# Optimization experiments

Measured on AMD Instinct MI355X. Metric: run time of the kernel, lower is better.

The kernel has to match this reference:

```python
import jax, jax.numpy as jnp
import numpy as np

NEG_INF = -1e30


def setup_inputs() -> dict:
    key = jax.random.key(0)
    kx, km, kq, kk, kv, ko = jax.random.split(key, 6)
    B, D, L = 2, 1024, 2048
    H, DK = 16, 64
    x = jax.random.normal(kx, (B, D, L), dtype=jnp.float32)
    mask = (jax.random.uniform(km, (B, L)) < 0.9).astype(jnp.float32)
    # per-head projection weights, stacked: (H, D, DK); output proj (D, H*DK)==(D, D)
    sq = 1.0 / np.sqrt(D)
    Wq = jax.random.normal(kq, (H, D, DK), dtype=jnp.float32) * sq
    Wk = jax.random.normal(kk, (H, D, DK), dtype=jnp.float32) * sq
    Wv = jax.random.normal(kv, (H, D, DK), dtype=jnp.float32) * sq
    Wo = jax.random.normal(ko, (D, H * DK), dtype=jnp.float32) * sq
    return {"x": x, "mask": mask, "Wq": Wq, "Wk": Wk, "Wv": Wv, "Wo": Wo}


def reference(x, mask, Wq, Wk, Wv, Wo):
    # x: (B, D, L); original transposes to (B, L, D)
    B, D, L = x.shape
    H, _, DK = Wq.shape
    xt = jnp.transpose(x, (0, 2, 1))  # (B, L, D)
    q = jnp.einsum('bld,hdk->bhlk', xt, Wq)
    k = jnp.einsum('bld,hdk->bhlk', xt, Wk)
    v = jnp.einsum('bld,hdk->bhlk', xt, Wv)
    scores = jnp.einsum('bhlk,bhmk->bhlm', q, k) * (1.0 / np.sqrt(DK))
    # masked log-softmax over keys (hmask), squad-style: mask*logit + (1-mask)*-1e30
    hmask = mask[:, None, None, :]  # (B,1,1,Lk)
    masked = hmask * scores + (1.0 - hmask) * NEG_INF
    logp = jax.nn.log_softmax(masked, axis=-1)
    # second softmax over the log-probs, then multiplicative vmask on query dim
    p = jax.nn.softmax(logp, axis=-1) * mask[:, None, :, None]
    heads = jnp.einsum('bhlm,bhmk->bhlk', p, v)  # (B,H,L,DK)
    head = jnp.transpose(heads, (0, 2, 1, 3)).reshape(B, L, H * DK)
    out = jnp.einsum('ble,de->bld', head, Wo)  # matmul(head, Wo) with Wo (D, H*DK)... 
    # NOTE: torch.matmul(head, Wo) treats Wo as (H*DK_in, D_out) only if square; here
    # Wo is (D, H*DK) with D == H*DK, and torch contracts head's last dim with Wo's FIRST dim:
    out = head @ Wo  # (B, L, H*DK) @ (D, H*DK) requires D==H*DK; contracts dim 0 of Wo
    return jnp.transpose(out, (0, 2, 1))  # (B, D, L)


if __name__ == "__main__":
    print(reference(**setup_inputs()).shape)
```

## Files before the change

kernel.cpp:

```cpp
#include <hip/hip_runtime.h>
#include <hip/hip_bf16.h>

typedef unsigned short u16;
typedef unsigned int u32;
typedef unsigned long long u64;
typedef short s8v __attribute__((ext_vector_type(8)));
typedef __bf16 bfv8 __attribute__((ext_vector_type(8)));
typedef float f4 __attribute__((ext_vector_type(4)));
typedef u64 u64v2 __attribute__((ext_vector_type(2)));

static constexpr int B = 2, D = 1024, L = 2048, H = 16, DK = 64, E = 1024;
static constexpr float QSCALE = 0.125f * 1.44269504088896340736f;
static constexpr float SMB = -16.0f;

#define DEV __device__ __forceinline__

DEV u16 f2bf(float f) {
  unsigned int u = __float_as_uint(f);
  u += 0x7FFFu + ((u >> 16) & 1u);
  return (u16)(u >> 16);
}
DEV float fexp2(float x) { return __builtin_amdgcn_exp2f(x); }
DEV u32 pkbf(float a, float b) {
  __hip_bfloat162 h = __float22bfloat162_rn(float2{a, b});
  u32 r;
  __builtin_memcpy(&r, &h, 4);
  return r;
}

#define GLD_LDS16(gp, lp)                                                     \
  __builtin_amdgcn_global_load_lds(                                           \
      (const __attribute__((address_space(1))) void*)(gp),                    \
      (__attribute__((address_space(3))) void*)(lp), 16, 0, 0)

__global__ __launch_bounds__(256) void k_prep(
    const float* __restrict__ x, const float* __restrict__ Wq,
    const float* __restrict__ Wk, const float* __restrict__ Wv,
    const float* __restrict__ Wo, u16* __restrict__ xt, u16* __restrict__ Wt,
    u16* __restrict__ WoT) {
  __shared__ u16 t[64][67];
  const int tid = threadIdx.x;
  const int g = blockIdx.x;
  const float* src;
  u16* dst;
  int sld, dld;
  if (g < 1024) {
    const int b = g >> 9, dt = (g >> 5) & 15, lt = g & 31;
    src = x + ((size_t)b * D + dt * 64) * L + lt * 64;
    sld = L;
    dst = xt + ((size_t)b * L + lt * 64) * D + dt * 64;
    dld = D;
  } else if (g < 1792) {
    const int u = g - 1024;
    const int w = u >> 8, h = (u >> 4) & 15, dt = u & 15;
    const float* Ws = (w == 0) ? Wq : ((w == 1) ? Wk : Wv);
    src = Ws + ((size_t)h * D + dt * 64) * DK;
    sld = DK;
    dst = Wt + ((size_t)(w * H + h) * DK) * D + dt * 64;
    dld = D;
  } else {
    const int v = g - 1792;
    const int et = v >> 4, dt = v & 15;
    src = Wo + ((size_t)et * 64) * D + dt * 64;
    sld = D;
    dst = WoT + ((size_t)dt * 64) * E + et * 64;
    dld = E;
  }
  const int r = tid >> 2, c16 = (tid & 3) * 16;
#pragma unroll
  for (int j = 0; j < 16; j += 4) {
    const f4 v4 = *(const f4*)(src + (size_t)r * sld + c16 + j);
    t[r][c16 + j]     = f2bf(v4[0]);
    t[r][c16 + j + 1] = f2bf(v4[1]);
    t[r][c16 + j + 2] = f2bf(v4[2]);
    t[r][c16 + j + 3] = f2bf(v4[3]);
  }
  __syncthreads();
  s8v o0, o1;
#pragma unroll
  for (int i = 0; i < 8; ++i) {
    o0[i] = (short)t[c16 + i][r];
    o1[i] = (short)t[c16 + 8 + i][r];
  }
  *(s8v*)(dst + (size_t)r * dld + c16)     = o0;
  *(s8v*)(dst + (size_t)r * dld + c16 + 8) = o1;
}

template <int AR>
DEV void gemm_tile(const u16* __restrict__ A, const u16* __restrict__ Bt,
                   int arow0, int brow0, u16* As, u16* Bs,
                   f4 (&acc)[AR / 32][4]) {
  const int tid = threadIdx.x;
  const int wid = tid >> 6, lane = tid & 63;
  const int q = lane >> 4, ln = lane & 15;
  const int wr = wid >> 1, wc = wid & 1;
  const int lrow = lane >> 2;
  const int lcg = (lane & 3) ^ ((lane >> 3) & 3);
  const int scA = (q ^ ((ln >> 1) & 3)) * 8;
  constexpr int MT = AR / 32;

  for (int k0 = 0; k0 < 1024; k0 += 32) {
    __syncthreads();
#pragma unroll
    for (int j = 0; j < AR / 64; ++j) {
      const int rb = wid * (AR / 4) + j * 16;
      const u16* gp = A + (size_t)(arow0 + rb + lrow) * 1024 + k0 + lcg * 8;
      GLD_LDS16(gp, As + rb * 32);
    }
#pragma unroll
    for (int j = 0; j < 2; ++j) {
      const int rb = wid * 32 + j * 16;
      const u16* gp = Bt + (size_t)(brow0 + rb + lrow) * 1024 + k0 + lcg * 8;
      GLD_LDS16(gp, Bs + rb * 32);
    }
    __syncthreads();
    bfv8 af[MT], bf[4];
#pragma unroll
    for (int mt = 0; mt < MT; ++mt)
      af[mt] = *(const bfv8*)(As + (wr * (AR / 2) + mt * 16 + ln) * 32 + scA);
#pragma unroll
    for (int nt = 0; nt < 4; ++nt)
      bf[nt] = *(const bfv8*)(Bs + (wc * 64 + nt * 16 + ln) * 32 + scA);
#pragma unroll
    for (int mt = 0; mt < MT; ++mt)
#pragma unroll
      for (int nt = 0; nt < 4; ++nt)
        acc[mt][nt] = __builtin_amdgcn_mfma_f32_16x16x32_bf16(
            af[mt], bf[nt], acc[mt][nt], 0, 0, 0);
  }
}

__global__ __launch_bounds__(256, 3) void k_qkvg(
    const u16* __restrict__ xt, const u16* __restrict__ Wt,
    u16* __restrict__ Q, u16* __restrict__ K, u16* __restrict__ Vt) {
  __shared__ u16 As[128 * 32];
  __shared__ u16 Bs[128 * 32];
  const int bm = blockIdx.x, bn = blockIdx.y;
  f4 acc[4][4];
#pragma unroll
  for (int mt = 0; mt < 4; ++mt)
#pragma unroll
    for (int nt = 0; nt < 4; ++nt) acc[mt][nt] = (f4){0.f, 0.f, 0.f, 0.f};
  gemm_tile<128>(xt, Wt, bm * 128, bn * 128, As, Bs, acc);

  const int tid = threadIdx.x, wid = tid >> 6, lane = tid & 63;
  const int q = lane >> 4, ln = lane & 15;
  const int wr = wid >> 1, wc = wid & 1;
  const int h2 = bn * 2 + wc;
  const int wsel = h2 >> 4, h = h2 & 15;
  const int b = bm >> 4;
  const int lbase = (bm & 15) * 128 + wr * 64;
  if (wsel == 0) {
    u16* dst = Q + (size_t)(b * H + h) * L * DK;
#pragma unroll
    for (int mt = 0; mt < 4; ++mt)
#pragma unroll
      for (int nt = 0; nt < 4; ++nt)
#pragma unroll
        for (int r = 0; r < 4; ++r)
          dst[(size_t)(lbase + mt * 16 + q * 4 + r) * DK + nt * 16 + ln] =
              f2bf(acc[mt][nt][r] * QSCALE);
  } else if (wsel == 1) {
    u16* dst = K + (size_t)(b * H + h) * L * DK;
#pragma unroll
    for (int mt = 0; mt < 4; ++mt)
#pragma unroll
      for (int nt = 0; nt < 4; ++nt)
#pragma unroll
        for (int r = 0; r < 4; ++r)
          dst[(size_t)(lbase + mt * 16 + q * 4 + r) * DK + nt * 16 + ln] =
              f2bf(acc[mt][nt][r]);
  } else {
    u16* dst = Vt + (size_t)(b * H + h) * DK * L;
#pragma unroll
    for (int mt = 0; mt < 4; ++mt)
#pragma unroll
      for (int nt = 0; nt < 4; ++nt)
#pragma unroll
        for (int r = 0; r < 4; ++r) {
          const int l = lbase + mt * 16 + q * 4 + r;
          dst[(size_t)(nt * 16 + ln) * L + (l & ~63) + ((l & 15) << 2) +
              ((l >> 4) & 3)] = f2bf(acc[mt][nt][r]);
        }
  }
}

__global__ __launch_bounds__(256, 2) void k_attn(
    const u16* __restrict__ Q, const u16* __restrict__ K,
    const u16* __restrict__ Vt, const float* __restrict__ mask,
    u16* __restrict__ Hd) {
  __shared__ u16 kt[64 * 64];
  __shared__ u16 vt[64 * 64];
  __shared__ float mf[L];
  __shared__ u16 p_lds[4][32 * 72];
  const int lt = blockIdx.x, h = blockIdx.y, b = blockIdx.z;
  const int tid = threadIdx.x;
  const int w = tid >> 6, lane = tid & 63, q = lane >> 4, ln = lane & 15;
  for (int i = tid; i < L; i += 256) mf[i] = mask[(size_t)b * L + i];

  const int bh = b * H + h;
  const u16* Qp = Q + (size_t)bh * L * DK;
  const u16* Kp = K + (size_t)bh * L * DK;
  const u16* Vp = Vt + (size_t)bh * DK * L;
  const int lq = lt * 128 + w * 32;

  bfv8 qf[2][2];
#pragma unroll
  for (int mt = 0; mt < 2; ++mt) {
    qf[mt][0] = *(const bfv8*)(Qp + (size_t)(lq + mt * 16 + ln) * DK + q * 8);
    qf[mt][1] =
        *(const bfv8*)(Qp + (size_t)(lq + mt * 16 + ln) * DK + 32 + q * 8);
  }

  f4 o[2][4];
  float l_r[2][4];
#pragma unroll
  for (int mt = 0; mt < 2; ++mt)
#pragma unroll
    for (int i = 0; i < 4; ++i) {
      o[mt][i] = (f4){0.f, 0.f, 0.f, 0.f};
      l_r[mt][i] = 0.f;
    }
  u16* pw = &p_lds[w][0];

  const int lrow = lane >> 3;
  const int lc = (lane & 7) ^ lrow;
  const int fr0 = w * 16 + lrow, fr1 = w * 16 + 8 + lrow;
  const int c0 = (q ^ (ln & 7)) * 8;
  const int c1 = ((q + 4) ^ (ln & 7)) * 8;

  for (int m0 = 0; m0 < L; m0 += 64) {
    __syncthreads();
    GLD_LDS16(Kp + (size_t)(m0 + fr0) * DK + lc * 8, kt + (w * 16) * 64);
    GLD_LDS16(Kp + (size_t)(m0 + fr1) * DK + lc * 8, kt + (w * 16 + 8) * 64);
    GLD_LDS16(Vp + (size_t)fr0 * L + m0 + lc * 8, vt + (w * 16) * 64);
    GLD_LDS16(Vp + (size_t)fr1 * L + m0 + lc * 8, vt + (w * 16 + 8) * 64);
    __syncthreads();

    float km[4];
    f4 s[2][4];
#pragma unroll
    for (int nt = 0; nt < 4; ++nt) {
      const int row = nt * 16 + ln;
      const bfv8 kf0 = *(const bfv8*)(kt + row * 64 + c0);
      const bfv8 kf1 = *(const bfv8*)(kt + row * 64 + c1);
      km[nt] = mf[m0 + row];
#pragma unroll
      for (int mt = 0; mt < 2; ++mt) {
        f4 a = (f4){SMB, SMB, SMB, SMB};
        a = __builtin_amdgcn_mfma_f32_16x16x32_bf16(qf[mt][0], kf0, a, 0, 0, 0);
        a = __builtin_amdgcn_mfma_f32_16x16x32_bf16(qf[mt][1], kf1, a, 0, 0, 0);
        s[mt][nt] = a;
      }
    }
#pragma unroll
    for (int mt = 0; mt < 2; ++mt)
#pragma unroll
      for (int r = 0; r < 4; ++r) {
        const float p0 = fexp2(s[mt][0][r]) * km[0];
        const float p1 = fexp2(s[mt][1][r]) * km[1];
        const float p2 = fexp2(s[mt][2][r]) * km[2];
        const float p3 = fexp2(s[mt][3][r]) * km[3];
        l_r[mt][r] += (p0 + p1) + (p2 + p3);
        const u64 pk = (u64)pkbf(p0, p1) | ((u64)pkbf(p2, p3) << 32);
        *(u64*)(pw + (mt * 16 + q * 4 + r) * 72 + ln * 4) = pk;
      }
    bfv8 pa[2][2];
#pragma unroll
    for (int mt = 0; mt < 2; ++mt) {
      u64v2 r0, r1;
      r0[0] = *(const u64*)(pw + (mt * 16 + ln) * 72 + q * 8);
      r0[1] = *(const u64*)(pw + (mt * 16 + ln) * 72 + q * 8 + 4);
      r1[0] = *(const u64*)(pw + (mt * 16 + ln) * 72 + 32 + q * 8);
      r1[1] = *(const u64*)(pw + (mt * 16 + ln) * 72 + 32 + q * 8 + 4);
      pa[mt][0] = __builtin_bit_cast(bfv8, r0);
      pa[mt][1] = __builtin_bit_cast(bfv8, r1);
    }
#pragma unroll
    for (int nt = 0; nt < 4; ++nt) {
      const int row = nt * 16 + ln;
      const bfv8 vf0 = *(const bfv8*)(vt + row * 64 + c0);
      const bfv8 vf1 = *(const bfv8*)(vt + row * 64 + c1);
#pragma unroll
      for (int mt = 0; mt < 2; ++mt) {
        o[mt][nt] = __builtin_amdgcn_mfma_f32_16x16x32_bf16(pa[mt][0], vf0,
                                                            o[mt][nt], 0, 0, 0);
        o[mt][nt] = __builtin_amdgcn_mfma_f32_16x16x32_bf16(pa[mt][1], vf1,
                                                            o[mt][nt], 0, 0, 0);
      }
    }
  }
#pragma unroll
  for (int mt = 0; mt < 2; ++mt)
#pragma unroll
    for (int r = 0; r < 4; ++r) {
#pragma unroll
      for (int off = 1; off < 16; off <<= 1)
        l_r[mt][r] += __shfl_xor(l_r[mt][r], off, 16);
      const float qm = mf[lq + mt * 16 + q * 4 + r];
      l_r[mt][r] = (qm != 0.0f) ? (1.0f / l_r[mt][r]) : 0.0f;
    }
#pragma unroll
  for (int mt = 0; mt < 2; ++mt)
#pragma unroll
    for (int nt = 0; nt < 4; ++nt)
#pragma unroll
      for (int r = 0; r < 4; ++r)
        Hd[(size_t)(b * L + lq + mt * 16 + q * 4 + r) * E + h * DK + nt * 16 +
           ln] = f2bf(o[mt][nt][r] * l_r[mt][r]);
}

__global__ __launch_bounds__(256, 2) void k_projg(const u16* __restrict__ WoT,
                                                  const u16* __restrict__ Hd,
                                                  float* __restrict__ out) {
  __shared__ u16 As[64 * 32];
  __shared__ u16 Bs[128 * 32];
  const int bm = blockIdx.x, bn = blockIdx.y;
  f4 acc[2][4];
#pragma unroll
  for (int mt = 0; mt < 2; ++mt)
#pragma unroll
    for (int nt = 0; nt < 4; ++nt) acc[mt][nt] = (f4){0.f, 0.f, 0.f, 0.f};
  gemm_tile<64>(WoT, Hd, bm * 64, bn * 128, As, Bs, acc);

  const int tid = threadIdx.x, wid = tid >> 6, lane = tid & 63;
  const int q = lane >> 4, ln = lane & 15;
  const int wr = wid >> 1, wc = wid & 1;
#pragma unroll
  for (int mt = 0; mt < 2; ++mt)
#pragma unroll
    for (int nt = 0; nt < 4; ++nt)
#pragma unroll
      for (int r = 0; r < 4; ++r) {
        const int d = bm * 64 + wr * 32 + mt * 16 + q * 4 + r;
        const int n = bn * 128 + wc * 64 + nt * 16 + ln;
        const int bb = n >> 11, l = n & 2047;
        out[((size_t)(bb * D + d)) * L + l] = acc[mt][nt][r];
      }
}

extern "C" void kernel_launch(void* const* d_in, const int* in_sizes, int n_in,
                              void* d_out, int out_size, void* d_ws,
                              size_t ws_size, hipStream_t stream) {
  const float* x    = (const float*)d_in[0];
  const float* mask = (const float*)d_in[1];
  const float* Wq   = (const float*)d_in[2];
  const float* Wk   = (const float*)d_in[3];
  const float* Wv   = (const float*)d_in[4];
  const float* Wo   = (const float*)d_in[5];
  u16* ws = (u16*)d_ws;
  u16* Qws  = ws;
  u16* Kws  = ws + 4194304;
  u16* Vtws = ws + 8388608;
  u16* WoTw = ws + 12582912;
  u16* Wtws = ws + 13631488;
  u16* xtws = ws + 16777216;
  u16* Hdws = ws + 16777216;

  k_prep<<<2048, 256, 0, stream>>>(x, Wq, Wk, Wv, Wo, xtws, Wtws, WoTw);
  k_qkvg<<<dim3(32, 24), 256, 0, stream>>>(xtws, Wtws, Qws, Kws, Vtws);
  k_attn<<<dim3(16, 16, 2), 256, 0, stream>>>(Qws, Kws, Vtws, mask, Hdws);
  k_projg<<<dim3(16, 32), 256, 0, stream>>>(WoTw, Hdws, (float*)d_out);
}
```

Before: 191.0 us.

## Double-buffer LDS tiles in GEMMs and attention; fold key mask into score bias

Both GEMM tile loops and the attention K/V loop now use two LDS buffers. The next tile's global-to-LDS loads are issued right after a single barrier, so they overlap with the MFMA work on the current tile, and one barrier per iteration is removed. The key mask becomes an additive bias (a large negative value) loaded as the initial MFMA accumulator, which drops the per-element multiply after exp2. The attention grid is reordered so heads vary fastest. Doubling LDS use may lower occupancy, and the bias trick depends on exp2 underflowing to zero for masked keys.

Measured after the change: 195.4 us. 2.3% more time.

```diff
diff --git a/kernel.cpp b/kernel.cpp
--- a/kernel.cpp
+++ b/kernel.cpp
@@ -12,6 +12,7 @@
 static constexpr int B = 2, D = 1024, L = 2048, H = 16, DK = 64, E = 1024;
 static constexpr float QSCALE = 0.125f * 1.44269504088896340736f;
 static constexpr float SMB = -16.0f;
+static constexpr float MASKB = -12000.0f;
 
 #define DEV __device__ __forceinline__
 
@@ -99,28 +100,34 @@
   const int scA = (q ^ ((ln >> 1) & 3)) * 8;
   constexpr int MT = AR / 32;
 
-  for (int k0 = 0; k0 < 1024; k0 += 32) {
-    __syncthreads();
+  auto issue = [&](int k0, int pb) {
 #pragma unroll
     for (int j = 0; j < AR / 64; ++j) {
       const int rb = wid * (AR / 4) + j * 16;
-      const u16* gp = A + (size_t)(arow0 + rb + lrow) * 1024 + k0 + lcg * 8;
-      GLD_LDS16(gp, As + rb * 32);
+      GLD_LDS16(A + (size_t)(arow0 + rb + lrow) * 1024 + k0 + lcg * 8,
+                As + pb * (AR * 32) + rb * 32);
     }
 #pragma unroll
     for (int j = 0; j < 2; ++j) {
       const int rb = wid * 32 + j * 16;
-      const u16* gp = Bt + (size_t)(brow0 + rb + lrow) * 1024 + k0 + lcg * 8;
-      GLD_LDS16(gp, Bs + rb * 32);
-    }
+      GLD_LDS16(Bt + (size_t)(brow0 + rb + lrow) * 1024 + k0 + lcg * 8,
+                Bs + pb * (128 * 32) + rb * 32);
+    }
+  };
+  issue(0, 0);
+  for (int it = 0; it < 32; ++it) {
     __syncthreads();
+    const int pb = it & 1;
+    if (it < 31) issue((it + 1) * 32, pb ^ 1);
+    const u16* Ab = As + pb * (AR * 32);
+    const u16* Bb = Bs + pb * (128 * 32);
     bfv8 af[MT], bf[4];
 #pragma unroll
     for (int mt = 0; mt < MT; ++mt)
-      af[mt] = *(const bfv8*)(As + (wr * (AR / 2) + mt * 16 + ln) * 32 + scA);
+      af[mt] = *(const bfv8*)(Ab + (wr * (AR / 2) + mt * 16 + ln) * 32 + scA);
 #pragma unroll
     for (int nt = 0; nt < 4; ++nt)
-      bf[nt] = *(const bfv8*)(Bs + (wc * 64 + nt * 16 + ln) * 32 + scA);
+      bf[nt] = *(const bfv8*)(Bb + (wc * 64 + nt * 16 + ln) * 32 + scA);
 #pragma unroll
     for (int mt = 0; mt < MT; ++mt)
 #pragma unroll
@@ -133,8 +140,8 @@
 __global__ __launch_bounds__(256, 3) void k_qkvg(
     const u16* __restrict__ xt, const u16* __restrict__ Wt,
     u16* __restrict__ Q, u16* __restrict__ K, u16* __restrict__ Vt) {
-  __shared__ u16 As[128 * 32];
-  __shared__ u16 Bs[128 * 32];
+  __shared__ u16 As[2 * 128 * 32];
+  __shared__ u16 Bs[2 * 128 * 32];
   const int bm = blockIdx.x, bn = blockIdx.y;
   f4 acc[4][4];
 #pragma unroll
@@ -189,14 +196,15 @@
     const u16* __restrict__ Q, const u16* __restrict__ K,
     const u16* __restrict__ Vt, const float* __restrict__ mask,
     u16* __restrict__ Hd) {
-  __shared__ u16 kt[64 * 64];
-  __shared__ u16 vt[64 * 64];
-  __shared__ float mf[L];
+  __shared__ u16 kt[2][64 * 64];
+  __shared__ u16 vt[2][64 * 64];
+  __shared__ float mb[L];
   __shared__ u16 p_lds[4][32 * 72];
-  const int lt = blockIdx.x, h = blockIdx.y, b = blockIdx.z;
+  const int h = blockIdx.x, lt = blockIdx.y, b = blockIdx.z;
   const int tid = threadIdx.x;
   const int w = tid >> 6, lane = tid & 63, q = lane >> 4, ln = lane & 15;
-  for (int i = tid; i < L; i += 256) mf[i] = mask[(size_t)b * L + i];
+  for (int i = tid; i < L; i += 256)
+    mb[i] = (mask[(size_t)b * L + i] != 0.0f) ? SMB : MASKB;
 
   const int bh = b * H + h;
   const u16* Qp = Q + (size_t)bh * L * DK;
@@ -212,6 +220,17 @@
         *(const bfv8*)(Qp + (size_t)(lq + mt * 16 + ln) * DK + 32 + q * 8);
   }
 
+  const int lrow = lane >> 3;
+  const int lc = (lane & 7) ^ lrow;
+  const int fr0 = w * 16 + lrow, fr1 = fr0 + 8;
+  const int c0 = (q ^ (ln & 7)) * 8;
+  const int c1 = ((q + 4) ^ (ln & 7)) * 8;
+
+  GLD_LDS16(Kp + (size_t)fr0 * DK + lc * 8, &kt[0][(w * 16) * 64]);
+  GLD_LDS16(Kp + (size_t)fr1 * DK + lc * 8, &kt[0][(w * 16 + 8) * 64]);
+  GLD_LDS16(Vp + (size_t)fr0 * L + lc * 8, &vt[0][(w * 16) * 64]);
+  GLD_LDS16(Vp + (size_t)fr1 * L + lc * 8, &vt[0][(w * 16 + 8) * 64]);
+
   f4 o[2][4];
   float l_r[2][4];
 #pragma unroll
@@ -223,31 +242,33 @@
     }
   u16* pw = &p_lds[w][0];
 
-  const int lrow = lane >> 3;
-  const int lc = (lane & 7) ^ lrow;
-  const int fr0 = w * 16 + lrow, fr1 = w * 16 + 8 + lrow;
-  const int c0 = (q ^ (ln & 7)) * 8;
-  const int c1 = ((q + 4) ^ (ln & 7)) * 8;
-
-  for (int m0 = 0; m0 < L; m0 += 64) {
+  for (int it = 0; it < L / 64; ++it) {
+    const int m0 = it * 64;
     __syncthreads();
-    GLD_LDS16(Kp + (size_t)(m0 + fr0) * DK + lc * 8, kt + (w * 16) * 64);
-    GLD_LDS16(Kp + (size_t)(m0 + fr1) * DK + lc * 8, kt + (w * 16 + 8) * 64);
-    GLD_LDS16(Vp + (size_t)fr0 * L + m0 + lc * 8, vt + (w * 16) * 64);
-    GLD_LDS16(Vp + (size_t)fr1 * L + m0 + lc * 8, vt + (w * 16 + 8) * 64);
-    __syncthreads();
-
-    float km[4];
+    const int cur = it & 1;
+    if (it + 1 < L / 64) {
+      const int nxt = cur ^ 1;
+      const int m1 = m0 + 64;
+      GLD_LDS16(Kp + (size_t)(m1 + fr0) * DK + lc * 8, &kt[nxt][(w * 16) * 64]);
+      GLD_LDS16(Kp + (size_t)(m1 + fr1) * DK + lc * 8,
+                &kt[nxt][(w * 16 + 8) * 64]);
+      GLD_LDS16(Vp + (size_t)fr0 * L + m1 + lc * 8, &vt[nxt][(w * 16) * 64]);
+      GLD_LDS16(Vp + (size_t)fr1 * L + m1 + lc * 8,
+                &vt[nxt][(w * 16 + 8) * 64]);
+    }
+    const u16* ktc = &kt[cur][0];
+    const u16* vtc = &vt[cur][0];
+
     f4 s[2][4];
 #pragma unroll
     for (int nt = 0; nt < 4; ++nt) {
       const int row = nt * 16 + ln;
-      const bfv8 kf0 = *(const bfv8*)(kt + row * 64 + c0);
-      const bfv8 kf1 = *(const bfv8*)(kt + row * 64 + c1);
-      km[nt] = mf[m0 + row];
+      const bfv8 kf0 = *(const bfv8*)(ktc + row * 64 + c0);
+      const bfv8 kf1 = *(const bfv8*)(ktc + row * 64 + c1);
+      const float mbv = mb[m0 + row];
 #pragma unroll
       for (int mt = 0; mt < 2; ++mt) {
-        f4 a = (f4){SMB, SMB, SMB, SMB};
+        f4 a = (f4){mbv, mbv, mbv, mbv};
         a = __builtin_amdgcn_mfma_f32_16x16x32_bf16(qf[mt][0], kf0, a, 0, 0, 0);
         a = __builtin_amdgcn_mfma_f32_16x16x32_bf16(qf[mt][1], kf1, a, 0, 0, 0);
         s[mt][nt] = a;
@@ -257,10 +278,10 @@
     for (int mt = 0; mt < 2; ++mt)
 #pragma unroll
       for (int r = 0; r < 4; ++r) {
-        const float p0 = fexp2(s[mt][0][r]) * km[0];
-        const float p1 = fexp2(s[mt][1][r]) * km[1];
-        const float p2 = fexp2(s[mt][2][r]) * km[2];
-        const float p3 = fexp2(s[mt][3][r]) * km[3];
+        const float p0 = fexp2(s[mt][0][r]);
+        const float p1 = fexp2(s[mt][1][r]);
+        const float p2 = fexp2(s[mt][2][r]);
+        const float p3 = fexp2(s[mt][3][r]);
         l_r[mt][r] += (p0 + p1) + (p2 + p3);
         const u64 pk = (u64)pkbf(p0, p1) | ((u64)pkbf(p2, p3) << 32);
         *(u64*)(pw + (mt * 16 + q * 4 + r) * 72 + ln * 4) = pk;
@@ -279,8 +300,8 @@
 #pragma unroll
     for (int nt = 0; nt < 4; ++nt) {
       const int row = nt * 16 + ln;
-      const bfv8 vf0 = *(const bfv8*)(vt + row * 64 + c0);
-      const bfv8 vf1 = *(const bfv8*)(vt + row * 64 + c1);
+      const bfv8 vf0 = *(const bfv8*)(vtc + row * 64 + c0);
+      const bfv8 vf1 = *(const bfv8*)(vtc + row * 64 + c1);
 #pragma unroll
       for (int mt = 0; mt < 2; ++mt) {
         o[mt][nt] = __builtin_amdgcn_mfma_f32_16x16x32_bf16(pa[mt][0], vf0,
@@ -297,8 +318,8 @@
 #pragma unroll
       for (int off = 1; off < 16; off <<= 1)
         l_r[mt][r] += __shfl_xor(l_r[mt][r], off, 16);
-      const float qm = mf[lq + mt * 16 + q * 4 + r];
-      l_r[mt][r] = (qm != 0.0f) ? (1.0f / l_r[mt][r]) : 0.0f;
+      const float qb = mb[lq + mt * 16 + q * 4 + r];
+      l_r[mt][r] = (qb > -100.0f) ? (1.0f / l_r[mt][r]) : 0.0f;
     }
 #pragma unroll
   for (int mt = 0; mt < 2; ++mt)
@@ -313,8 +334,8 @@
 __global__ __launch_bounds__(256, 2) void k_projg(const u16* __restrict__ WoT,
                                                   const u16* __restrict__ Hd,
                                                   float* __restrict__ out) {
-  __shared__ u16 As[64 * 32];
-  __shared__ u16 Bs[128 * 32];
+  __shared__ u16 As[2 * 64 * 32];
+  __shared__ u16 Bs[2 * 128 * 32];
   const int bm = blockIdx.x, bn = blockIdx.y;
   f4 acc[2][4];
 #pragma unroll
```

## Software-pipeline attention loop with double/triple-buffered K/V and mask-as-bias

Applied to the files above, without the earlier changes.

The attention kernel now prefetches the next K/V tile into separate LDS buffers (two for K, three for V) while computing, and interleaves the QK of tile i with the softmax and PV of tile i-1, so there is one barrier per iteration instead of two. The key mask is folded into the MFMA accumulator initialisation as a large negative bias instead of a multiply after exp. The grid is reordered so heads vary fastest, which may change L2 reuse of the shared mask and inputs. The extra buffers raise LDS use and register pressure, which could hurt occupancy at two blocks per CU.

New measurement: 191.4 us. No clear change (+0.2%).

```diff
diff --git a/kernel.cpp b/kernel.cpp
--- a/kernel.cpp
+++ b/kernel.cpp
@@ -12,6 +12,7 @@
 static constexpr int B = 2, D = 1024, L = 2048, H = 16, DK = 64, E = 1024;
 static constexpr float QSCALE = 0.125f * 1.44269504088896340736f;
 static constexpr float SMB = -16.0f;
+static constexpr float MASKB = -12000.0f;
 
 #define DEV __device__ __forceinline__
 
@@ -104,14 +105,14 @@
 #pragma unroll
     for (int j = 0; j < AR / 64; ++j) {
       const int rb = wid * (AR / 4) + j * 16;
-      const u16* gp = A + (size_t)(arow0 + rb + lrow) * 1024 + k0 + lcg * 8;
-      GLD_LDS16(gp, As + rb * 32);
+      GLD_LDS16(A + (size_t)(arow0 + rb + lrow) * 1024 + k0 + lcg * 8,
+                As + rb * 32);
     }
 #pragma unroll
     for (int j = 0; j < 2; ++j) {
       const int rb = wid * 32 + j * 16;
-      const u16* gp = Bt + (size_t)(brow0 + rb + lrow) * 1024 + k0 + lcg * 8;
-      GLD_LDS16(gp, Bs + rb * 32);
+      GLD_LDS16(Bt + (size_t)(brow0 + rb + lrow) * 1024 + k0 + lcg * 8,
+                Bs + rb * 32);
     }
     __syncthreads();
     bfv8 af[MT], bf[4];
@@ -189,14 +190,15 @@
     const u16* __restrict__ Q, const u16* __restrict__ K,
     const u16* __restrict__ Vt, const float* __restrict__ mask,
     u16* __restrict__ Hd) {
-  __shared__ u16 kt[64 * 64];
-  __shared__ u16 vt[64 * 64];
-  __shared__ float mf[L];
+  __shared__ u16 kt[2][64 * 64];
+  __shared__ u16 vt[3][64 * 64];
+  __shared__ float mb[L];
   __shared__ u16 p_lds[4][32 * 72];
-  const int lt = blockIdx.x, h = blockIdx.y, b = blockIdx.z;
+  const int h = blockIdx.x, lt = blockIdx.y, b = blockIdx.z;
   const int tid = threadIdx.x;
   const int w = tid >> 6, lane = tid & 63, q = lane >> 4, ln = lane & 15;
-  for (int i = tid; i < L; i += 256) mf[i] = mask[(size_t)b * L + i];
+  for (int i = tid; i < L; i += 256)
+    mb[i] = (mask[(size_t)b * L + i] != 0.0f) ? SMB : MASKB;
 
   const int bh = b * H + h;
   const u16* Qp = Q + (size_t)bh * L * DK;
@@ -212,6 +214,20 @@
         *(const bfv8*)(Qp + (size_t)(lq + mt * 16 + ln) * DK + 32 + q * 8);
   }
 
+  const int lrow = lane >> 3;
+  const int lc = (lane & 7) ^ lrow;
+  const int fr0 = w * 16 + lrow, fr1 = fr0 + 8;
+  const int c0 = (q ^ (ln & 7)) * 8;
+  const int c1 = ((q + 4) ^ (ln & 7)) * 8;
+
+  auto stage = [&](int m0, int kb, int vb) {
+    GLD_LDS16(Kp + (size_t)(m0 + fr0) * DK + lc * 8, &kt[kb][(w * 16) * 64]);
+    GLD_LDS16(Kp + (size_t)(m0 + fr1) * DK + lc * 8,
+              &kt[kb][(w * 16 + 8) * 64]);
+    GLD_LDS16(Vp + (size_t)fr0 * L + m0 + lc * 8, &vt[vb][(w * 16) * 64]);
+    GLD_LDS16(Vp + (size_t)fr1 * L + m0 + lc * 8, &vt[vb][(w * 16 + 8) * 64]);
+  };
+
   f4 o[2][4];
   float l_r[2][4];
 #pragma unroll
@@ -222,49 +238,47 @@
       l_r[mt][i] = 0.f;
     }
   u16* pw = &p_lds[w][0];
-
-  const int lrow = lane >> 3;
-  const int lc = (lane & 7) ^ lrow;
-  const int fr0 = w * 16 + lrow, fr1 = w * 16 + 8 + lrow;
-  const int c0 = (q ^ (ln & 7)) * 8;
-  const int c1 = ((q + 4) ^ (ln & 7)) * 8;
-
-  for (int m0 = 0; m0 < L; m0 += 64) {
-    __syncthreads();
-    GLD_LDS16(Kp + (size_t)(m0 + fr0) * DK + lc * 8, kt + (w * 16) * 64);
-    GLD_LDS16(Kp + (size_t)(m0 + fr1) * DK + lc * 8, kt + (w * 16 + 8) * 64);
-    GLD_LDS16(Vp + (size_t)fr0 * L + m0 + lc * 8, vt + (w * 16) * 64);
-    GLD_LDS16(Vp + (size_t)fr1 * L + m0 + lc * 8, vt + (w * 16 + 8) * 64);
-    __syncthreads();
-
-    float km[4];
-    f4 s[2][4];
+  f4 sp[2][4];
+
+  auto qk = [&](int m0, int kb) {
+    const u16* ktc = &kt[kb][0];
+    bfv8 kf0[4], kf1[4];
+    float mbv[4];
 #pragma unroll
     for (int nt = 0; nt < 4; ++nt) {
       const int row = nt * 16 + ln;
-      const bfv8 kf0 = *(const bfv8*)(kt + row * 64 + c0);
-      const bfv8 kf1 = *(const bfv8*)(kt + row * 64 + c1);
-      km[nt] = mf[m0 + row];
+      kf0[nt] = *(const bfv8*)(ktc + row * 64 + c0);
+      kf1[nt] = *(const bfv8*)(ktc + row * 64 + c1);
+      mbv[nt] = mb[m0 + row];
+    }
+#pragma unroll
+    for (int nt = 0; nt < 4; ++nt)
 #pragma unroll
       for (int mt = 0; mt < 2; ++mt) {
-        f4 a = (f4){SMB, SMB, SMB, SMB};
-        a = __builtin_amdgcn_mfma_f32_16x16x32_bf16(qf[mt][0], kf0, a, 0, 0, 0);
-        a = __builtin_amdgcn_mfma_f32_16x16x32_bf16(qf[mt][1], kf1, a, 0, 0, 0);
-        s[mt][nt] = a;
+        f4 a = (f4){mbv[nt], mbv[nt], mbv[nt], mbv[nt]};
+        a = __builtin_amdgcn_mfma_f32_16x16x32_bf16(qf[mt][0], kf0[nt], a, 0,
+                                                    0, 0);
+        a = __builtin_amdgcn_mfma_f32_16x16x32_bf16(qf[mt][1], kf1[nt], a, 0,
+                                                    0, 0);
+        sp[mt][nt] = a;
       }
-    }
+  };
+  auto softmax_p = [&]() {
 #pragma unroll
     for (int mt = 0; mt < 2; ++mt)
 #pragma unroll
       for (int r = 0; r < 4; ++r) {
-        const float p0 = fexp2(s[mt][0][r]) * km[0];
-        const float p1 = fexp2(s[mt][1][r]) * km[1];
-        const float p2 = fexp2(s[mt][2][r]) * km[2];
-        const float p3 = fexp2(s[mt][3][r]) * km[3];
+        const float p0 = fexp2(sp[mt][0][r]);
+        const float p1 = fexp2(sp[mt][1][r]);
+        const float p2 = fexp2(sp[mt][2][r]);
+        const float p3 = fexp2(sp[mt][3][r]);
         l_r[mt][r] += (p0 + p1) + (p2 + p3);
         const u64 pk = (u64)pkbf(p0, p1) | ((u64)pkbf(p2, p3) << 32);
         *(u64*)(pw + (mt * 16 + q * 4 + r) * 72 + ln * 4) = pk;
       }
+  };
+  auto pv = [&](int vb) {
+    const u16* vtc = &vt[vb][0];
     bfv8 pa[2][2];
 #pragma unroll
     for (int mt = 0; mt < 2; ++mt) {
@@ -279,8 +293,8 @@
 #pragma unroll
     for (int nt = 0; nt < 4; ++nt) {
       const int row = nt * 16 + ln;
-      const bfv8 vf0 = *(const bfv8*)(vt + row * 64 + c0);
-      const bfv8 vf1 = *(const bfv8*)(vt + row * 64 + c1);
+      const bfv8 vf0 = *(const bfv8*)(vtc + row * 64 + c0);
+      const bfv8 vf1 = *(const bfv8*)(vtc + row * 64 + c1);
 #pragma unroll
       for (int mt = 0; mt < 2; ++mt) {
         o[mt][nt] = __builtin_amdgcn_mfma_f32_16x16x32_bf16(pa[mt][0], vf0,
@@ -289,7 +303,23 @@
                                                             o[mt][nt], 0, 0, 0);
       }
     }
-  }
+  };
+
+  stage(0, 0, 0);
+  __syncthreads();
+  stage(64, 1, 1);
+  qk(0, 0);
+
+  for (int it = 1; it < L / 64; ++it) {
+    __syncthreads();
+    if (it + 1 < L / 64) stage((it + 1) * 64, (it + 1) & 1, (it + 1) % 3);
+    softmax_p();
+    qk(it * 64, it & 1);
+    pv((it - 1) % 3);
+  }
+  softmax_p();
+  pv((L / 64 - 1) % 3);
+
 #pragma unroll
   for (int mt = 0; mt < 2; ++mt)
 #pragma unroll
@@ -297,8 +327,8 @@
 #pragma unroll
       for (int off = 1; off < 16; off <<= 1)
         l_r[mt][r] += __shfl_xor(l_r[mt][r], off, 16);
-      const float qm = mf[lq + mt * 16 + q * 4 + r];
-      l_r[mt][r] = (qm != 0.0f) ? (1.0f / l_r[mt][r]) : 0.0f;
+      const float qb = mb[lq + mt * 16 + q * 4 + r];
+      l_r[mt][r] = (qb > -100.0f) ? (1.0f / l_r[mt][r]) : 0.0f;
     }
 #pragma unroll
   for (int mt = 0; mt < 2; ++mt)
```
